# Kernel tuning notes

Measured on AMD Instinct MI355X. Metric: run time of the kernel, lower is better.

Reference implementation:

```python
import jax, jax.numpy as jnp
import numpy as np

V, E, H, C = 50000, 300, 512, 3
B, P_LEN, H_LEN = 64, 128, 64


def _lstm(x, Wih, Whh, bih, bhh, h0, c0):
    """torch-style LSTM (gate order i,f,g,o). x: [B,T,E] -> outputs [B,T,H], hT, cT."""
    def step(carry, xt):
        h, c = carry
        g = xt @ Wih.T + h @ Whh.T + bih + bhh  # [B,4H]
        i, f, gg, o = jnp.split(g, 4, axis=-1)
        c = jax.nn.sigmoid(f) * c + jax.nn.sigmoid(i) * jnp.tanh(gg)
        h = jax.nn.sigmoid(o) * jnp.tanh(c)
        return (h, c), h
    (hT, cT), ys = jax.lax.scan(step, (h0, c0), jnp.swapaxes(x, 0, 1))
    return jnp.swapaxes(ys, 0, 1), hT, cT


def setup_inputs() -> dict:
    key = jax.random.key(0)
    ks = iter(jax.random.split(key, 32))
    n = lambda shape, s=0.05: jax.random.normal(next(ks), shape, dtype=jnp.float32) * s
    inp = {
        "premise": jax.random.randint(next(ks), (B, P_LEN), 0, V, dtype=jnp.int32),
        "hypothesis": jax.random.randint(next(ks), (B, H_LEN), 0, V, dtype=jnp.int32),
        "emb": n((V, E), 0.1),
        "Wih1": n((4 * H, E)), "Whh1": n((4 * H, H)), "bih1": n((4 * H,)), "bhh1": n((4 * H,)),
        "Wih2": n((4 * H, E)), "Whh2": n((4 * H, H)), "bih2": n((4 * H,)), "bhh2": n((4 * H,)),
        "W_y": n((H, H)), "W_h": n((H, H)), "W_r": n((H, H)), "W_t": n((H, H)),
        "w_att": n((1, H)),
        "fc1_w": n((H, H)), "fc1_b": n((H,)),
        "fc2_w": n((H, H)), "fc2_b": n((H,)),
        "fc3_w": n((C, H)), "fc3_b": n((C,)),
    }
    return inp


def reference(premise, hypothesis, emb,
              Wih1, Whh1, bih1, bhh1,
              Wih2, Whh2, bih2, bhh2,
              W_y, W_h, W_r, W_t, w_att,
              fc1_w, fc1_b, fc2_w, fc2_b, fc3_w, fc3_b):
    Bsz = premise.shape[0]
    Hd = Whh1.shape[1]
    zeros = jnp.zeros((Bsz, Hd), jnp.float32)

    # premise LSTM
    xp = emb[premise]                                   # [B,P,E]
    out_p, _, c_p = _lstm(xp, Wih1, Whh1, bih1, bhh1, zeros, zeros)
    # hypothesis LSTM initialized with (h0=0, c0=c_p)
    xh = emb[hypothesis]                                # [B,Th,E]
    out_h, hn_h, _ = _lstm(xh, Wih2, Whh2, bih2, bhh2, zeros, c_p)

    # word-by-word attention: a1 = W_y @ V^T, fixed across steps
    a1 = jnp.einsum('hj,bpj->bhp', W_y, out_p)          # [B,H,P]
    wv = w_att[0]                                       # [H]

    def att_step(r, q_t):
        # r: [B,H] attention state; q_t: [B,H] hypothesis step
        a2 = q_t @ W_h.T + r @ W_r.T                    # [B,H]
        s = jnp.einsum('h,bhp->bp', wv, jnp.tanh(a1 + a2[:, :, None]))
        scores = jax.nn.softmax(s, axis=-1)             # over premise positions
        r = jnp.einsum('bph,bp->bh', out_p, scores) + jnp.tanh(r @ W_t.T)
        return r, None

    r, _ = jax.lax.scan(att_step, zeros, jnp.swapaxes(out_h, 0, 1))

    rep = jnp.tanh(r @ fc1_w.T + fc1_b + hn_h @ fc2_w.T + fc2_b)
    return rep @ fc3_w.T + fc3_b                         # [B,C]
```

## Files before the change

kernel.cpp:

```cpp
#include <hip/hip_runtime.h>
#include <math.h>

#define BSZ 64
#define PLEN 128
#define HLEN 64
#define EDIM 300
#define HDIM 512
#define G4 2048
#define NCLS 3

#define SPIN_CAP (1 << 18)

#define CR16 576
#define C16(f) ((((f) >> 5) * 36) + ((f) & 31))

__device__ __forceinline__ float sigf(float x) { return 1.0f / (1.0f + __expf(-x)); }
__device__ __forceinline__ float tanhfast(float x) { return 1.0f - 2.0f / (__expf(2.0f * x) + 1.0f); }

__device__ __forceinline__ unsigned long long aload64(const unsigned long long* p) {
    return __hip_atomic_load(p, __ATOMIC_RELAXED, __HIP_MEMORY_SCOPE_AGENT);
}
__device__ __forceinline__ void astore64(unsigned long long* p, unsigned long long v) {
    __hip_atomic_store(p, v, __ATOMIC_RELAXED, __HIP_MEMORY_SCOPE_AGENT);
}
__device__ __forceinline__ unsigned long long fpack2(float lo, float hi) {
    float2 v = make_float2(lo, hi);
    return *(unsigned long long*)&v;
}
__device__ __forceinline__ float2 funpack2(unsigned long long u) {
    union { unsigned long long u; float2 f; } c; c.u = u; return c.f;
}

__global__ __launch_bounds__(256) void ws_zero(unsigned long long* p) {
    p[(size_t)blockIdx.x * 256 + threadIdx.x] = 0ull;
}

__global__ __launch_bounds__(256) void proj_kernel(
    const int* __restrict__ toks, const float* __restrict__ emb,
    const float* __restrict__ Wih, const float* __restrict__ bih,
    const float* __restrict__ bhh, float* __restrict__ out)
{
    __shared__ float es[32 * 100];
    __shared__ float wsh[64 * 100];
    __shared__ int tks[32];
    const int m0 = blockIdx.x * 32, r0 = blockIdx.y * 64;
    const int tid = threadIdx.x;
    const int tx = tid & 15, ty = tid >> 4;
    float acc[2][4] = {{0.f, 0.f, 0.f, 0.f}, {0.f, 0.f, 0.f, 0.f}};
    if (tid < 32) tks[tid] = toks[m0 + tid];
    __syncthreads();
    for (int kc = 0; kc < 3; kc++) {
        if (kc) __syncthreads();
        for (int i = tid; i < 800; i += 256) {
            int row = i / 25, k4 = i % 25;
            ((float4*)es)[i] = ((const float4*)(emb + (size_t)tks[row] * EDIM + kc * 100))[k4];
        }
        for (int i = tid; i < 1600; i += 256) {
            int row = i / 25, k4 = i % 25;
            ((float4*)wsh)[i] = ((const float4*)(Wih + (size_t)(r0 + row) * EDIM + kc * 100))[k4];
        }
        __syncthreads();
        const float4* e0 = (const float4*)es + ty * 25;
        const float4* e1 = e0 + 16 * 25;
        const float4* w0 = (const float4*)wsh + tx * 25;
#pragma unroll
        for (int k = 0; k < 25; k++) {
            float4 ea = e0[k], eb = e1[k];
#pragma unroll
            for (int j = 0; j < 4; j++) {
                float4 w = w0[k + j * 400];
                acc[0][j] += ea.x * w.x + ea.y * w.y + ea.z * w.z + ea.w * w.w;
                acc[1][j] += eb.x * w.x + eb.y * w.y + eb.z * w.z + eb.w * w.w;
            }
        }
    }
#pragma unroll
    for (int j = 0; j < 4; j++) {
        int rr = r0 + tx + j * 16;
        float bsum = bih[rr] + bhh[rr];
        out[(size_t)(m0 + ty) * G4 + rr]      = acc[0][j] + bsum;
        out[(size_t)(m0 + ty + 16) * G4 + rr] = acc[1][j] + bsum;
    }
}

__global__ __launch_bounds__(256, 1) void lstm_coop(
    const float* __restrict__ xp, const float* __restrict__ xh,
    const float* __restrict__ Whh1, const float* __restrict__ Whh2,
    float* __restrict__ outp, float* __restrict__ outh,
    unsigned long long* __restrict__ hA, unsigned long long* __restrict__ hB,
    unsigned long long* __restrict__ hC, unsigned long long* __restrict__ hD,
    unsigned long long* __restrict__ doneH)
{
    const int tid = threadIdx.x;
    const int ug = blockIdx.x >> 3;
    const int bg = blockIdx.x & 7;
    const int u0 = ug * 16, b0 = bg * 8;
    const int rq = tid >> 4, cc = tid & 15;

    __shared__ __align__(16) float hst[8 * CR16];
    __shared__ float gsm[64][9];

    float4 w4[32];
#pragma unroll
    for (int j = 0; j < 4; j++) {
        int rr = 4 * rq + j;
        const float4* src = (const float4*)(Whh1 +
            ((size_t)((rr >> 4) * HDIM + u0 + (rr & 15))) * HDIM) + cc * 8;
#pragma unroll
        for (int q = 0; q < 8; q++) w4[j * 8 + q] = src[q];
    }
    float creg = 0.0f;
    const int bbc = tid >> 4, uuc = tid & 15;
    unsigned long long* dn = doneH + bg * 32;

    for (int t = 0; t < PLEN + HLEN; t++) {
        const int layer2 = (t >= PLEN) ? 1 : 0;
        const int tloc = layer2 ? t - PLEN : t;
        const int T = layer2 ? HLEN : PLEN;
        const float* xproj = layer2 ? xh : xp;
        float* outseq = layer2 ? outh : outp;
        unsigned long long* wA = layer2 ? hC : hA;
        unsigned long long* wB = layer2 ? hD : hB;
        unsigned long long* hwr = (t & 1) ? wB : wA;
        const unsigned long long* hrd = (t & 1) ? wA : wB;

        float gi = 0.f, gf = 0.f, gg = 0.f, go = 0.f;
        if (tid < 128) {
            size_t xb = ((size_t)(b0 + bbc) * T + tloc) * G4 + u0 + uuc;
            gi = xproj[xb];        gf = xproj[xb + 512];
            gg = xproj[xb + 1024]; go = xproj[xb + 1536];
        }

        if (t == PLEN) {
#pragma unroll
            for (int j = 0; j < 4; j++) {
                int rr = 4 * rq + j;
                const float4* src = (const float4*)(Whh2 +
                    ((size_t)((rr >> 4) * HDIM + u0 + (rr & 15))) * HDIM) + cc * 8;
#pragma unroll
                for (int q = 0; q < 8; q++) w4[j * 8 + q] = src[q];
            }
        }
        const bool have_h = (tloc != 0);
        if (have_h) {
            if (tid < 32) {
                unsigned long long v = aload64(dn + tid);
                int guard = 0;
                while (!__all(v >= (unsigned long long)t)) {
                    if (++guard > SPIN_CAP) break;
                    __builtin_amdgcn_s_sleep(1);
                    if (v < (unsigned long long)t) v = aload64(dn + tid);
                }
            }
            __syncthreads();
            __asm__ volatile("" ::: "memory");
            const unsigned long long* src = hrd + (size_t)b0 * 256;
            unsigned long long v[8];
#pragma unroll
            for (int i = 0; i < 8; i++) v[i] = aload64(src + tid + i * 256);
#pragma unroll
            for (int i = 0; i < 8; i++) {
                int idx = tid + i * 256;
                int bb = idx >> 8, j = idx & 255;
                float2 f = funpack2(v[i]);
                *(float2*)&hst[bb * CR16 + C16(2 * j)] = f;
            }
            __syncthreads();
#pragma unroll 1
            for (int bb = 0; bb < 8; bb++) {
                const float* hb = &hst[bb * CR16 + cc * 36];
                float a0 = 0.f, a1 = 0.f, a2 = 0.f, a3 = 0.f;
#pragma unroll
                for (int q = 0; q < 8; q++) {
                    float4 hv = *(const float4*)(hb + 4 * q);
                    float4 x;
                    x = w4[q];      a0 += x.x * hv.x + x.y * hv.y + x.z * hv.z + x.w * hv.w;
                    x = w4[8 + q];  a1 += x.x * hv.x + x.y * hv.y + x.z * hv.z + x.w * hv.w;
                    x = w4[16 + q]; a2 += x.x * hv.x + x.y * hv.y + x.z * hv.z + x.w * hv.w;
                    x = w4[24 + q]; a3 += x.x * hv.x + x.y * hv.y + x.z * hv.z + x.w * hv.w;
                }
#pragma unroll
                for (int o = 1; o < 16; o <<= 1) {
                    a0 += __shfl_xor(a0, o);
                    a1 += __shfl_xor(a1, o);
                    a2 += __shfl_xor(a2, o);
                    a3 += __shfl_xor(a3, o);
                }
                if (cc == 0) {
                    gsm[4 * rq + 0][bb] = a0;
                    gsm[4 * rq + 1][bb] = a1;
                    gsm[4 * rq + 2][bb] = a2;
                    gsm[4 * rq + 3][bb] = a3;
                }
            }
        }
        __syncthreads();
        float hn = 0.f;
        if (tid < 128) {
            if (have_h) {
                gi += gsm[uuc][bbc];
                gf += gsm[16 + uuc][bbc];
                gg += gsm[32 + uuc][bbc];
                go += gsm[48 + uuc][bbc];
            }
            float cn = sigf(gf) * creg + sigf(gi) * tanhfast(gg);
            hn = sigf(go) * tanhfast(cn);
            creg = cn;
            float pr = __shfl_xor(hn, 1);
            if ((uuc & 1) == 0)
                astore64(hwr + (size_t)(b0 + bbc) * 256 + (u0 + uuc) / 2, fpack2(hn, pr));
        }
        __asm__ volatile("s_waitcnt vmcnt(0)" ::: "memory");
        __syncthreads();
        if (tid == 0) astore64(&dn[ug], (unsigned long long)(t + 1));
        if (tid < 128)
            outseq[((size_t)(b0 + bbc) * T + tloc) * HDIM + u0 + uuc] = hn;
    }
}

__global__ __launch_bounds__(256) void a1_kernel(
    const float* __restrict__ W, const float* __restrict__ src,
    float* __restrict__ dst, int T)
{
    __shared__ float os[32 * 132];
    __shared__ float wsh[64 * 132];
    const int b = blockIdx.x, p0 = blockIdx.y * 32, h0 = blockIdx.z * 64;
    const int tid = threadIdx.x;
    const int tx = tid & 15, ty = tid >> 4;
    float acc[2][4] = {{0.f, 0.f, 0.f, 0.f}, {0.f, 0.f, 0.f, 0.f}};
    for (int kc = 0; kc < 4; kc++) {
        if (kc) __syncthreads();
        for (int i = tid; i < 1024; i += 256) {
            int row = i >> 5, k4 = i & 31;
            ((float4*)os)[row * 33 + k4] =
                ((const float4*)(src + ((size_t)(b * T) + p0 + row) * HDIM + kc * 128))[k4];
        }
        for (int i = tid; i < 2048; i += 256) {
            int row = i >> 5, k4 = i & 31;
            ((float4*)wsh)[row * 33 + k4] =
                ((const float4*)(W + (size_t)(h0 + row) * HDIM + kc * 128))[k4];
        }
        __syncthreads();
        const float4* o0 = (const float4*)os + ty * 33;
        const float4* o1 = o0 + 16 * 33;
        const float4* w0 = (const float4*)wsh + tx * 33;
#pragma unroll
        for (int k = 0; k < 32; k++) {
            float4 ea = o0[k], eb = o1[k];
#pragma unroll
            for (int j = 0; j < 4; j++) {
                float4 w = w0[k + j * 528];
                acc[0][j] += ea.x * w.x + ea.y * w.y + ea.z * w.z + ea.w * w.w;
                acc[1][j] += eb.x * w.x + eb.y * w.y + eb.z * w.z + eb.w * w.w;
            }
        }
    }
#pragma unroll
    for (int j = 0; j < 4; j++) {
        int hh = h0 + tx + j * 16;
        dst[((size_t)b * T + p0 + ty) * HDIM + hh]      = acc[0][j];
        dst[((size_t)b * T + p0 + ty + 16) * HDIM + hh] = acc[1][j];
    }
}

#define OSTR 2056
__global__ __launch_bounds__(256, 1) void att_coop2(
    const float* __restrict__ a1b,
    const float* __restrict__ a2qb,
    const float* __restrict__ outp,
    const float* __restrict__ Wr, const float* __restrict__ Wt,
    const float* __restrict__ wv,
    unsigned long long* __restrict__ rA, unsigned long long* __restrict__ rB,
    unsigned long long* __restrict__ sPart,
    unsigned long long* __restrict__ dnS, unsigned long long* __restrict__ dnR)
{
    const int tid = threadIdx.x;
    const int ug = blockIdx.x >> 3;
    const int bg = blockIdx.x & 7;
    const int u0 = ug * 16, b0 = bg * 8;
    const int rp = tid >> 4, cc = tid & 15;
    const int ab = tid >> 5, aq = tid & 31;

    __shared__ __align__(16) float rst[8 * CR16];
    __shared__ __align__(16) float ops[8 * OSTR];
    __shared__ __align__(16) float scst[8][132];
    __shared__ float a2sl[16][9];
    __shared__ float ttsl[16][9];
    __shared__ float wvs[16];

    float4 wr4[8], wt4[8];
    {
        const float4* sr = (const float4*)(Wr + (size_t)(u0 + rp) * HDIM) + cc * 8;
        const float4* st = (const float4*)(Wt + (size_t)(u0 + rp) * HDIM) + cc * 8;
#pragma unroll
        for (int q = 0; q < 8; q++) { wr4[q] = sr[q]; wt4[q] = st[q]; }
    }
    if (tid < 16) wvs[tid] = wv[u0 + tid];

    for (int i = tid; i < 8 * 128 * 4; i += 256) {
        int bb = i >> 9;
        int rem = i & 511;
        int p = rem >> 2, q = rem & 3;
        float4 v = *((const float4*)(outp + ((size_t)(b0 + bb) * PLEN + p) * HDIM + u0) + q);
        *((float4*)(ops + bb * OSTR + p * 16) + q) = v;
    }
    float4 a1r[4][4];
#pragma unroll
    for (int p = 0; p < 4; p++) {
        const float4* src = (const float4*)(a1b +
            ((size_t)(b0 + ab) * PLEN + 4 * aq + p) * HDIM + u0);
#pragma unroll
        for (int k = 0; k < 4; k++) a1r[p][k] = src[k];
    }
    __syncthreads();

    unsigned long long* myS = dnS + bg * 32;
    unsigned long long* myR = dnR + bg * 32;
    const int bbc = tid >> 4, uuc = tid & 15;

    for (int t = 0; t < HLEN; t++) {
        unsigned long long* rwr = (t & 1) ? rB : rA;
        const unsigned long long* rrd = (t & 1) ? rA : rB;
        unsigned long long* sp = sPart + ((size_t)((t & 1) * 8 + bg)) * 16384;

        if (tid < 128) {
            int b = tid >> 4, hh = tid & 15;
            a2sl[hh][b] = a2qb[((size_t)(b0 + b) * HLEN + t) * HDIM + u0 + hh];
            ttsl[hh][b] = 0.f;
        }
        if (t > 0) {
            if (tid < 32) {
                unsigned long long v = aload64(myR + tid);
                int guard = 0;
                while (!__all(v >= (unsigned long long)t)) {
                    if (++guard > SPIN_CAP) break;
                    __builtin_amdgcn_s_sleep(1);
                    if (v < (unsigned long long)t) v = aload64(myR + tid);
                }
            }
            __syncthreads();
            __asm__ volatile("" ::: "memory");
            const unsigned long long* src = rrd + (size_t)b0 * 256;
            unsigned long long v[8];
#pragma unroll
            for (int i = 0; i < 8; i++) v[i] = aload64(src + tid + i * 256);
#pragma unroll
            for (int i = 0; i < 8; i++) {
                int idx = tid + i * 256;
                int bb = idx >> 8, j = idx & 255;
                float2 f = funpack2(v[i]);
                *(float2*)&rst[bb * CR16 + C16(2 * j)] = f;
            }
        }
        __syncthreads();
        if (t > 0) {
#pragma unroll 1
            for (int b = 0; b < 8; b++) {
                const float* hb = &rst[b * CR16 + cc * 36];
                float ar = 0.f, at = 0.f;
#pragma unroll
                for (int q = 0; q < 8; q++) {
                    float4 hv = *(const float4*)(hb + 4 * q);
                    float4 x = wr4[q], y = wt4[q];
                    ar += x.x * hv.x + x.y * hv.y + x.z * hv.z + x.w * hv.w;
                    at += y.x * hv.x + y.y * hv.y + y.z * hv.z + y.w * hv.w;
                }
#pragma unroll
                for (int o = 1; o < 16; o <<= 1) {
                    ar += __shfl_xor(ar, o);
                    at += __shfl_xor(at, o);
                }
                if (cc == 0) {
                    a2sl[rp][b] += ar;
                    ttsl[rp][b] = tanhfast(at);
                }
            }
        }
        __syncthreads();
        {
            float s4[4];
#pragma unroll
            for (int p = 0; p < 4; p++) {
                float s = 0.f;
#pragma unroll
                for (int k = 0; k < 4; k++) {
                    float4 av = a1r[p][k];
                    s += wvs[4 * k + 0] * tanhfast(av.x + a2sl[4 * k + 0][ab])
                       + wvs[4 * k + 1] * tanhfast(av.y + a2sl[4 * k + 1][ab])
                       + wvs[4 * k + 2] * tanhfast(av.z + a2sl[4 * k + 2][ab])
                       + wvs[4 * k + 3] * tanhfast(av.w + a2sl[4 * k + 3][ab]);
                }
                s4[p] = s;
            }
            unsigned long long* d = sp + ((size_t)ug * 8 + ab) * 64 + aq * 2;
            astore64(d, fpack2(s4[0], s4[1]));
            astore64(d + 1, fpack2(s4[2], s4[3]));
        }
        __asm__ volatile("s_waitcnt vmcnt(0)" ::: "memory");
        __syncthreads();
        if (tid == 0) astore64(&myS[ug], (unsigned long long)(t + 1));

        {
            if (tid < 32) {
                unsigned long long v = aload64(myS + tid);
                int guard = 0;
                while (!__all(v >= (unsigned long long)(t + 1))) {
                    if (++guard > SPIN_CAP) break;
                    __builtin_amdgcn_s_sleep(1);
                    if (v < (unsigned long long)(t + 1)) v = aload64(myS + tid);
                }
            }
            __syncthreads();
            __asm__ volatile("" ::: "memory");
#pragma unroll
            for (int i = 0; i < 2; i++) {
                int idx = tid + i * 256;
                int b = idx >> 6, p2 = idx & 63;
                float sx = 0.f, sy = 0.f;
#pragma unroll 8
                for (int g = 0; g < 32; g++) {
                    float2 f = funpack2(aload64(sp + ((size_t)g * 8 + b) * 64 + p2));
                    sx += f.x; sy += f.y;
                }
                scst[b][2 * p2] = sx;
                scst[b][2 * p2 + 1] = sy;
            }
        }
        __syncthreads();
        {
            const int bb = tid >> 5, j = tid & 31;
            float4 v = *(float4*)&scst[bb][j * 4];
            float mx = fmaxf(fmaxf(v.x, v.y), fmaxf(v.z, v.w));
#pragma unroll
            for (int o = 1; o < 32; o <<= 1) mx = fmaxf(mx, __shfl_xor(mx, o));
            float ex = __expf(v.x - mx), ey = __expf(v.y - mx);
            float ez = __expf(v.z - mx), ew = __expf(v.w - mx);
            float ssum = (ex + ey) + (ez + ew);
#pragma unroll
            for (int o = 1; o < 32; o <<= 1) ssum += __shfl_xor(ssum, o);
            float inv = 1.0f / ssum;
            float4 sc4 = make_float4(ex * inv, ey * inv, ez * inv, ew * inv);
            *(float4*)&scst[bb][j * 4] = sc4;
        }
        __syncthreads();
        if (tid < 128) {
            float acc = ttsl[uuc][bbc];
            const float* opb = ops + bbc * OSTR + uuc;
#pragma unroll 8
            for (int p = 0; p < PLEN; p++)
                acc += scst[bbc][p] * opb[p * 16];
            float pr = __shfl_xor(acc, 1);
            if ((uuc & 1) == 0)
                astore64(rwr + (size_t)(b0 + bbc) * 256 + (u0 + uuc) / 2, fpack2(acc, pr));
        }
        __asm__ volatile("s_waitcnt vmcnt(0)" ::: "memory");
        __syncthreads();
        if (tid == 0) astore64(&myR[ug], (unsigned long long)(t + 1));
    }
}

__global__ __launch_bounds__(256) void final_kernel(
    const unsigned long long* __restrict__ r2, const float* __restrict__ outh,
    const float* __restrict__ fc1w, const float* __restrict__ fc1b,
    const float* __restrict__ fc2w, const float* __restrict__ fc2b,
    const float* __restrict__ fc3w, const float* __restrict__ fc3b,
    float* __restrict__ out)
{
    int b = blockIdx.x, tid = threadIdx.x;
    __shared__ float rs[HDIM], hs[HDIM], rep[HDIM], red[256];
    {
        float2 f = funpack2(r2[(size_t)b * 256 + tid]);
        rs[2 * tid] = f.x; rs[2 * tid + 1] = f.y;
    }
    for (int i = tid; i < 128; i += 256)
        ((float4*)hs)[i] = ((const float4*)(outh + ((size_t)(b * HLEN + HLEN - 1)) * HDIM))[i];
    __syncthreads();
    for (int u = tid; u < HDIM; u += 256) {
        const float4* w1 = (const float4*)(fc1w + (size_t)u * HDIM);
        const float4* w2 = (const float4*)(fc2w + (size_t)u * HDIM);
        float a = 0.f, bacc = 0.f;
        for (int k = 0; k < 128; k++) {
            float4 rv = ((float4*)rs)[k], hv = ((float4*)hs)[k];
            float4 x = w1[k]; a    += rv.x * x.x + rv.y * x.y + rv.z * x.z + rv.w * x.w;
            float4 y = w2[k]; bacc += hv.x * y.x + hv.y * y.y + hv.z * y.z + hv.w * y.w;
        }
        rep[u] = tanhfast(a + fc1b[u] + bacc + fc2b[u]);
    }
    __syncthreads();
    for (int cix = 0; cix < NCLS; cix++) {
        red[tid] = rep[tid] * fc3w[(size_t)cix * HDIM + tid]
                 + rep[tid + 256] * fc3w[(size_t)cix * HDIM + tid + 256];
        __syncthreads();
        for (int off = 128; off; off >>= 1) {
            if (tid < off) red[tid] += red[tid + off];
            __syncthreads();
        }
        if (tid == 0) out[b * NCLS + cix] = red[0] + fc3b[cix];
        __syncthreads();
    }
}

extern "C" void kernel_launch(void* const* d_in, const int* in_sizes, int n_in,
                              void* d_out, int out_size, void* d_ws, size_t ws_size,
                              hipStream_t stream)
{
    const int*   premise = (const int*)d_in[0];
    const int*   hyp     = (const int*)d_in[1];
    const float* emb     = (const float*)d_in[2];
    const float* Wih1    = (const float*)d_in[3];
    const float* Whh1    = (const float*)d_in[4];
    const float* bih1    = (const float*)d_in[5];
    const float* bhh1    = (const float*)d_in[6];
    const float* Wih2    = (const float*)d_in[7];
    const float* Whh2    = (const float*)d_in[8];
    const float* bih2    = (const float*)d_in[9];
    const float* bhh2    = (const float*)d_in[10];
    const float* Wy      = (const float*)d_in[11];
    const float* Wh      = (const float*)d_in[12];
    const float* Wr      = (const float*)d_in[13];
    const float* Wt      = (const float*)d_in[14];
    const float* wv      = (const float*)d_in[15];
    const float* fc1w    = (const float*)d_in[16];
    const float* fc1b    = (const float*)d_in[17];
    const float* fc2w    = (const float*)d_in[18];
    const float* fc2b    = (const float*)d_in[19];
    const float* fc3w    = (const float*)d_in[20];
    const float* fc3b    = (const float*)d_in[21];
    float* out = (float*)d_out;

    float* ws = (float*)d_ws;
    size_t off = 0;
    float* xp    = ws + off; off += (size_t)BSZ * PLEN * G4;
    float* xh    = ws + off; off += (size_t)BSZ * HLEN * G4;
    float* outp  = ws + off; off += (size_t)BSZ * PLEN * HDIM;
    float* outhp = ws + off; off += (size_t)BSZ * HLEN * HDIM;
    float* a1b   = ws + off; off += (size_t)BSZ * HDIM * PLEN;
    float* a2qb  = xp;
    unsigned long long* tbase = (unsigned long long*)(ws + off);
    unsigned long long* hAb   = tbase;
    unsigned long long* hBb   = tbase + 16384;
    unsigned long long* hCb   = tbase + 2 * 16384;
    unsigned long long* hDb   = tbase + 3 * 16384;
    unsigned long long* sPart = tbase + 4 * 16384;
    unsigned long long* dnH   = sPart + 262144;
    unsigned long long* dnS   = dnH + 256;
    unsigned long long* dnR   = dnS + 256;
    off += (size_t)(4 * 16384 + 262144 + 768) * 2;
    if (ws_size < off * sizeof(float)) return;

    ws_zero<<<dim3(3), dim3(256), 0, stream>>>(dnH);

    proj_kernel<<<dim3(BSZ * PLEN / 32, G4 / 64), dim3(256), 0, stream>>>(
        premise, emb, Wih1, bih1, bhh1, xp);
    proj_kernel<<<dim3(BSZ * HLEN / 32, G4 / 64), dim3(256), 0, stream>>>(
        hyp, emb, Wih2, bih2, bhh2, xh);

    lstm_coop<<<dim3(256), dim3(256), 0, stream>>>(
        xp, xh, Whh1, Whh2, outp, outhp, hAb, hBb, hCb, hDb, dnH);

    a1_kernel<<<dim3(BSZ, PLEN / 32, HDIM / 64), dim3(256), 0, stream>>>(
        Wy, outp, a1b, PLEN);
    a1_kernel<<<dim3(BSZ, HLEN / 32, HDIM / 64), dim3(256), 0, stream>>>(
        Wh, outhp, a2qb, HLEN);

    att_coop2<<<dim3(256), dim3(256), 0, stream>>>(
        a1b, a2qb, outp, Wr, Wt, wv, hCb, hDb, sPart, dnS, dnR);

    final_kernel<<<dim3(BSZ), dim3(256), 0, stream>>>(
        hDb, outhp, fc1w, fc1b, fc2w, fc2b, fc3w, fc3b, out);
}
```

Before: 3.141 ms.

## Fuse LSTM and attention into one persistent kernel with streamed a1/a2 computation

New measurement: 3.233 ms. 2.9% more time.

```diff
diff --git a/kernel.cpp b/kernel.cpp
--- a/kernel.cpp
+++ b/kernel.cpp
@@ -21,6 +21,12 @@
     return __hip_atomic_load(p, __ATOMIC_RELAXED, __HIP_MEMORY_SCOPE_AGENT);
 }
 __device__ __forceinline__ void astore64(unsigned long long* p, unsigned long long v) {
+    __hip_atomic_store(p, v, __ATOMIC_RELAXED, __HIP_MEMORY_SCOPE_AGENT);
+}
+__device__ __forceinline__ float aload32f(const float* p) {
+    return __hip_atomic_load(p, __ATOMIC_RELAXED, __HIP_MEMORY_SCOPE_AGENT);
+}
+__device__ __forceinline__ void astore32f(float* p, float v) {
     __hip_atomic_store(p, v, __ATOMIC_RELAXED, __HIP_MEMORY_SCOPE_AGENT);
 }
 __device__ __forceinline__ unsigned long long fpack2(float lo, float hi) {
@@ -83,263 +89,275 @@
     }
 }
 
-__global__ __launch_bounds__(256, 1) void lstm_coop(
+__global__ __launch_bounds__(256, 2) void fused_coop(
     const float* __restrict__ xp, const float* __restrict__ xh,
     const float* __restrict__ Whh1, const float* __restrict__ Whh2,
     float* __restrict__ outp, float* __restrict__ outh,
     unsigned long long* __restrict__ hA, unsigned long long* __restrict__ hB,
     unsigned long long* __restrict__ hC, unsigned long long* __restrict__ hD,
-    unsigned long long* __restrict__ doneH)
-{
-    const int tid = threadIdx.x;
-    const int ug = blockIdx.x >> 3;
-    const int bg = blockIdx.x & 7;
-    const int u0 = ug * 16, b0 = bg * 8;
-    const int rq = tid >> 4, cc = tid & 15;
-
-    __shared__ __align__(16) float hst[8 * CR16];
-    __shared__ float gsm[64][9];
-
-    float4 w4[32];
-#pragma unroll
-    for (int j = 0; j < 4; j++) {
-        int rr = 4 * rq + j;
-        const float4* src = (const float4*)(Whh1 +
-            ((size_t)((rr >> 4) * HDIM + u0 + (rr & 15))) * HDIM) + cc * 8;
-#pragma unroll
-        for (int q = 0; q < 8; q++) w4[j * 8 + q] = src[q];
-    }
-    float creg = 0.0f;
-    const int bbc = tid >> 4, uuc = tid & 15;
-    unsigned long long* dn = doneH + bg * 32;
-
-    for (int t = 0; t < PLEN + HLEN; t++) {
-        const int layer2 = (t >= PLEN) ? 1 : 0;
-        const int tloc = layer2 ? t - PLEN : t;
-        const int T = layer2 ? HLEN : PLEN;
-        const float* xproj = layer2 ? xh : xp;
-        float* outseq = layer2 ? outh : outp;
-        unsigned long long* wA = layer2 ? hC : hA;
-        unsigned long long* wB = layer2 ? hD : hB;
-        unsigned long long* hwr = (t & 1) ? wB : wA;
-        const unsigned long long* hrd = (t & 1) ? wA : wB;
-
-        float gi = 0.f, gf = 0.f, gg = 0.f, go = 0.f;
-        if (tid < 128) {
-            size_t xb = ((size_t)(b0 + bbc) * T + tloc) * G4 + u0 + uuc;
-            gi = xproj[xb];        gf = xproj[xb + 512];
-            gg = xproj[xb + 1024]; go = xproj[xb + 1536];
-        }
-
-        if (t == PLEN) {
-#pragma unroll
-            for (int j = 0; j < 4; j++) {
-                int rr = 4 * rq + j;
-                const float4* src = (const float4*)(Whh2 +
-                    ((size_t)((rr >> 4) * HDIM + u0 + (rr & 15))) * HDIM) + cc * 8;
-#pragma unroll
-                for (int q = 0; q < 8; q++) w4[j * 8 + q] = src[q];
-            }
-        }
-        const bool have_h = (tloc != 0);
-        if (have_h) {
-            if (tid < 32) {
-                unsigned long long v = aload64(dn + tid);
-                int guard = 0;
-                while (!__all(v >= (unsigned long long)t)) {
-                    if (++guard > SPIN_CAP) break;
-                    __builtin_amdgcn_s_sleep(1);
-                    if (v < (unsigned long long)t) v = aload64(dn + tid);
-                }
-            }
-            __syncthreads();
-            __asm__ volatile("" ::: "memory");
-            const unsigned long long* src = hrd + (size_t)b0 * 256;
-            unsigned long long v[8];
-#pragma unroll
-            for (int i = 0; i < 8; i++) v[i] = aload64(src + tid + i * 256);
-#pragma unroll
-            for (int i = 0; i < 8; i++) {
-                int idx = tid + i * 256;
-                int bb = idx >> 8, j = idx & 255;
-                float2 f = funpack2(v[i]);
-                *(float2*)&hst[bb * CR16 + C16(2 * j)] = f;
-            }
-            __syncthreads();
-#pragma unroll 1
-            for (int bb = 0; bb < 8; bb++) {
-                const float* hb = &hst[bb * CR16 + cc * 36];
-                float a0 = 0.f, a1 = 0.f, a2 = 0.f, a3 = 0.f;
-#pragma unroll
-                for (int q = 0; q < 8; q++) {
-                    float4 hv = *(const float4*)(hb + 4 * q);
-                    float4 x;
-                    x = w4[q];      a0 += x.x * hv.x + x.y * hv.y + x.z * hv.z + x.w * hv.w;
-                    x = w4[8 + q];  a1 += x.x * hv.x + x.y * hv.y + x.z * hv.z + x.w * hv.w;
-                    x = w4[16 + q]; a2 += x.x * hv.x + x.y * hv.y + x.z * hv.z + x.w * hv.w;
-                    x = w4[24 + q]; a3 += x.x * hv.x + x.y * hv.y + x.z * hv.z + x.w * hv.w;
-                }
-#pragma unroll
-                for (int o = 1; o < 16; o <<= 1) {
-                    a0 += __shfl_xor(a0, o);
-                    a1 += __shfl_xor(a1, o);
-                    a2 += __shfl_xor(a2, o);
-                    a3 += __shfl_xor(a3, o);
-                }
-                if (cc == 0) {
-                    gsm[4 * rq + 0][bb] = a0;
-                    gsm[4 * rq + 1][bb] = a1;
-                    gsm[4 * rq + 2][bb] = a2;
-                    gsm[4 * rq + 3][bb] = a3;
-                }
-            }
-        }
-        __syncthreads();
-        float hn = 0.f;
-        if (tid < 128) {
-            if (have_h) {
-                gi += gsm[uuc][bbc];
-                gf += gsm[16 + uuc][bbc];
-                gg += gsm[32 + uuc][bbc];
-                go += gsm[48 + uuc][bbc];
-            }
-            float cn = sigf(gf) * creg + sigf(gi) * tanhfast(gg);
-            hn = sigf(go) * tanhfast(cn);
-            creg = cn;
-            float pr = __shfl_xor(hn, 1);
-            if ((uuc & 1) == 0)
-                astore64(hwr + (size_t)(b0 + bbc) * 256 + (u0 + uuc) / 2, fpack2(hn, pr));
-        }
-        __asm__ volatile("s_waitcnt vmcnt(0)" ::: "memory");
-        __syncthreads();
-        if (tid == 0) astore64(&dn[ug], (unsigned long long)(t + 1));
-        if (tid < 128)
-            outseq[((size_t)(b0 + bbc) * T + tloc) * HDIM + u0 + uuc] = hn;
-    }
-}
-
-__global__ __launch_bounds__(256) void a1_kernel(
-    const float* __restrict__ W, const float* __restrict__ src,
-    float* __restrict__ dst, int T)
-{
-    __shared__ float os[32 * 132];
-    __shared__ float wsh[64 * 132];
-    const int b = blockIdx.x, p0 = blockIdx.y * 32, h0 = blockIdx.z * 64;
-    const int tid = threadIdx.x;
-    const int tx = tid & 15, ty = tid >> 4;
-    float acc[2][4] = {{0.f, 0.f, 0.f, 0.f}, {0.f, 0.f, 0.f, 0.f}};
-    for (int kc = 0; kc < 4; kc++) {
-        if (kc) __syncthreads();
-        for (int i = tid; i < 1024; i += 256) {
-            int row = i >> 5, k4 = i & 31;
-            ((float4*)os)[row * 33 + k4] =
-                ((const float4*)(src + ((size_t)(b * T) + p0 + row) * HDIM + kc * 128))[k4];
-        }
-        for (int i = tid; i < 2048; i += 256) {
-            int row = i >> 5, k4 = i & 31;
-            ((float4*)wsh)[row * 33 + k4] =
-                ((const float4*)(W + (size_t)(h0 + row) * HDIM + kc * 128))[k4];
-        }
-        __syncthreads();
-        const float4* o0 = (const float4*)os + ty * 33;
-        const float4* o1 = o0 + 16 * 33;
-        const float4* w0 = (const float4*)wsh + tx * 33;
-#pragma unroll
-        for (int k = 0; k < 32; k++) {
-            float4 ea = o0[k], eb = o1[k];
-#pragma unroll
-            for (int j = 0; j < 4; j++) {
-                float4 w = w0[k + j * 528];
-                acc[0][j] += ea.x * w.x + ea.y * w.y + ea.z * w.z + ea.w * w.w;
-                acc[1][j] += eb.x * w.x + eb.y * w.y + eb.z * w.z + eb.w * w.w;
-            }
-        }
-    }
-#pragma unroll
-    for (int j = 0; j < 4; j++) {
-        int hh = h0 + tx + j * 16;
-        dst[((size_t)b * T + p0 + ty) * HDIM + hh]      = acc[0][j];
-        dst[((size_t)b * T + p0 + ty + 16) * HDIM + hh] = acc[1][j];
-    }
-}
-
-#define OSTR 2056
-__global__ __launch_bounds__(256, 1) void att_coop2(
-    const float* __restrict__ a1b,
-    const float* __restrict__ a2qb,
-    const float* __restrict__ outp,
-    const float* __restrict__ Wr, const float* __restrict__ Wt,
+    unsigned long long* __restrict__ doneH,
+    float* __restrict__ a1b,
+    const float* __restrict__ Wh, const float* __restrict__ Wr,
+    const float* __restrict__ Wt, const float* __restrict__ Wy,
     const float* __restrict__ wv,
     unsigned long long* __restrict__ rA, unsigned long long* __restrict__ rB,
     unsigned long long* __restrict__ sPart,
     unsigned long long* __restrict__ dnS, unsigned long long* __restrict__ dnR)
 {
+    extern __shared__ __align__(16) float smem[];
     const int tid = threadIdx.x;
-    const int ug = blockIdx.x >> 3;
-    const int bg = blockIdx.x & 7;
+
+    if (blockIdx.x < 256) {
+        const int ug = blockIdx.x >> 3;
+        const int bg = blockIdx.x & 7;
+        const int u0 = ug * 16, b0 = bg * 8;
+        const int rq = tid >> 4, cc = tid & 15;
+
+        float* hst = smem;
+        float* gsm = smem + 8 * CR16;
+
+        float4 w4[32];
+#pragma unroll
+        for (int j = 0; j < 4; j++) {
+            int rr = 4 * rq + j;
+            const float4* src = (const float4*)(Whh1 +
+                ((size_t)((rr >> 4) * HDIM + u0 + (rr & 15))) * HDIM) + cc * 8;
+#pragma unroll
+            for (int q = 0; q < 8; q++) w4[j * 8 + q] = src[q];
+        }
+        float creg = 0.0f;
+        const int bbc = tid >> 4, uuc = tid & 15;
+        unsigned long long* dn = doneH + bg * 32;
+
+        for (int t = 0; t < PLEN + HLEN; t++) {
+            const int layer2 = (t >= PLEN) ? 1 : 0;
+            const int tloc = layer2 ? t - PLEN : t;
+            const int T = layer2 ? HLEN : PLEN;
+            const float* xproj = layer2 ? xh : xp;
+            float* outseq = layer2 ? outh : outp;
+            unsigned long long* wA = layer2 ? hC : hA;
+            unsigned long long* wB = layer2 ? hD : hB;
+            unsigned long long* hwr = (t & 1) ? wB : wA;
+            const unsigned long long* hrd = (t & 1) ? wA : wB;
+
+            float gi = 0.f, gf = 0.f, gg = 0.f, go = 0.f;
+            if (tid < 128) {
+                size_t xb = ((size_t)(b0 + bbc) * T + tloc) * G4 + u0 + uuc;
+                gi = xproj[xb];        gf = xproj[xb + 512];
+                gg = xproj[xb + 1024]; go = xproj[xb + 1536];
+            }
+            if (t == PLEN) {
+#pragma unroll
+                for (int j = 0; j < 4; j++) {
+                    int rr = 4 * rq + j;
+                    const float4* src = (const float4*)(Whh2 +
+                        ((size_t)((rr >> 4) * HDIM + u0 + (rr & 15))) * HDIM) + cc * 8;
+#pragma unroll
+                    for (int q = 0; q < 8; q++) w4[j * 8 + q] = src[q];
+                }
+            }
+            const bool have_h = (tloc != 0);
+            if (have_h) {
+                if (tid < 32) {
+                    unsigned long long v = aload64(dn + tid);
+                    int guard = 0;
+                    while (!__all(v >= (unsigned long long)t)) {
+                        if (++guard > SPIN_CAP) break;
+                        __builtin_amdgcn_s_sleep(1);
+                        if (v < (unsigned long long)t) v = aload64(dn + tid);
+                    }
+                }
+                __syncthreads();
+                __asm__ volatile("" ::: "memory");
+                const unsigned long long* src = hrd + (size_t)b0 * 256;
+                unsigned long long v[8];
+#pragma unroll
+                for (int i = 0; i < 8; i++) v[i] = aload64(src + tid + i * 256);
+#pragma unroll
+                for (int i = 0; i < 8; i++) {
+                    int idx = tid + i * 256;
+                    int bb = idx >> 8, j = idx & 255;
+                    float2 f = funpack2(v[i]);
+                    *(float2*)&hst[bb * CR16 + C16(2 * j)] = f;
+                }
+                __syncthreads();
+#pragma unroll 1
+                for (int bb = 0; bb < 8; bb++) {
+                    const float* hb = &hst[bb * CR16 + cc * 36];
+                    float a0 = 0.f, a1 = 0.f, a2 = 0.f, a3 = 0.f;
+#pragma unroll
+                    for (int q = 0; q < 8; q++) {
+                        float4 hv = *(const float4*)(hb + 4 * q);
+                        float4 x;
+                        x = w4[q];      a0 += x.x * hv.x + x.y * hv.y + x.z * hv.z + x.w * hv.w;
+                        x = w4[8 + q];  a1 += x.x * hv.x + x.y * hv.y + x.z * hv.z + x.w * hv.w;
+                        x = w4[16 + q]; a2 += x.x * hv.x + x.y * hv.y + x.z * hv.z + x.w * hv.w;
+                        x = w4[24 + q]; a3 += x.x * hv.x + x.y * hv.y + x.z * hv.z + x.w * hv.w;
+                    }
+#pragma unroll
+                    for (int o = 1; o < 16; o <<= 1) {
+                        a0 += __shfl_xor(a0, o);
+                        a1 += __shfl_xor(a1, o);
+                        a2 += __shfl_xor(a2, o);
+                        a3 += __shfl_xor(a3, o);
+                    }
+                    if (cc == 0) {
+                        gsm[(4 * rq + 0) * 9 + bb] = a0;
+                        gsm[(4 * rq + 1) * 9 + bb] = a1;
+                        gsm[(4 * rq + 2) * 9 + bb] = a2;
+                        gsm[(4 * rq + 3) * 9 + bb] = a3;
+                    }
+                }
+            }
+            __syncthreads();
+            if (tid < 128) {
+                if (have_h) {
+                    gi += gsm[uuc * 9 + bbc];
+                    gf += gsm[(16 + uuc) * 9 + bbc];
+                    gg += gsm[(32 + uuc) * 9 + bbc];
+                    go += gsm[(48 + uuc) * 9 + bbc];
+                }
+                float cn = sigf(gf) * creg + sigf(gi) * tanhfast(gg);
+                float hn = sigf(go) * tanhfast(cn);
+                creg = cn;
+                float pr = __shfl_xor(hn, 1);
+                if ((uuc & 1) == 0)
+                    astore64(hwr + (size_t)(b0 + bbc) * 256 + (u0 + uuc) / 2, fpack2(hn, pr));
+                astore32f(outseq + ((size_t)(b0 + bbc) * T + tloc) * HDIM + u0 + uuc, hn);
+            }
+            __asm__ volatile("s_waitcnt vmcnt(0)" ::: "memory");
+            __syncthreads();
+            if (tid == 0) astore64(&dn[ug], (unsigned long long)(t + 1));
+        }
+        return;
+    }
+
+    const int local = blockIdx.x - 256;
+    const int ug = local >> 3;
+    const int bg = local & 7;
     const int u0 = ug * 16, b0 = bg * 8;
     const int rp = tid >> 4, cc = tid & 15;
     const int ab = tid >> 5, aq = tid & 31;
 
-    __shared__ __align__(16) float rst[8 * CR16];
-    __shared__ __align__(16) float ops[8 * OSTR];
-    __shared__ __align__(16) float scst[8][132];
-    __shared__ float a2sl[16][9];
-    __shared__ float ttsl[16][9];
-    __shared__ float wvs[16];
-
-    float4 wr4[8], wt4[8];
+    float* qst  = smem;
+    float* rst  = smem + 4608;
+    float* scst = smem + 9216;
+    float* a2sl = smem + 10272;
+    float* ttsl = smem + 10416;
+    float* wvs  = smem + 10560;
+    float* psum = smem + 10576;
+
+    float4 wh4[8], wr4[8], wt4[8];
     {
+        const float4* sh = (const float4*)(Wh + (size_t)(u0 + rp) * HDIM) + cc * 8;
         const float4* sr = (const float4*)(Wr + (size_t)(u0 + rp) * HDIM) + cc * 8;
         const float4* st = (const float4*)(Wt + (size_t)(u0 + rp) * HDIM) + cc * 8;
 #pragma unroll
-        for (int q = 0; q < 8; q++) { wr4[q] = sr[q]; wt4[q] = st[q]; }
+        for (int q = 0; q < 8; q++) { wh4[q] = sh[q]; wr4[q] = sr[q]; wt4[q] = st[q]; }
     }
     if (tid < 16) wvs[tid] = wv[u0 + tid];
 
-    for (int i = tid; i < 8 * 128 * 4; i += 256) {
-        int bb = i >> 9;
-        int rem = i & 511;
-        int p = rem >> 2, q = rem & 3;
-        float4 v = *((const float4*)(outp + ((size_t)(b0 + bb) * PLEN + p) * HDIM + u0) + q);
-        *((float4*)(ops + bb * OSTR + p * 16) + q) = v;
-    }
-    float4 a1r[4][4];
-#pragma unroll
-    for (int p = 0; p < 4; p++) {
-        const float4* src = (const float4*)(a1b +
-            ((size_t)(b0 + ab) * PLEN + 4 * aq + p) * HDIM + u0);
-#pragma unroll
-        for (int k = 0; k < 4; k++) a1r[p][k] = src[k];
-    }
-    __syncthreads();
-
+    unsigned long long* dnl = doneH + bg * 32;
     unsigned long long* myS = dnS + bg * 32;
     unsigned long long* myR = dnR + bg * 32;
     const int bbc = tid >> 4, uuc = tid & 15;
+
+    {
+        float4 wy4[8];
+        const float4* sy = (const float4*)(Wy + (size_t)(u0 + rp) * HDIM) + cc * 8;
+#pragma unroll
+        for (int q = 0; q < 8; q++) wy4[q] = sy[q];
+
+        for (int p = 0; p < PLEN; p++) {
+            if (tid < 32) {
+                unsigned long long v = aload64(dnl + tid);
+                int guard = 0;
+                while (!__all(v >= (unsigned long long)(p + 1))) {
+                    if (++guard > SPIN_CAP) break;
+                    __builtin_amdgcn_s_sleep(1);
+                    if (v < (unsigned long long)(p + 1)) v = aload64(dnl + tid);
+                }
+            }
+            __syncthreads();
+            __asm__ volatile("" ::: "memory");
+            {
+                const unsigned long long* src =
+                    (const unsigned long long*)(outp) + ((size_t)b0 * PLEN + p) * 256;
+#pragma unroll
+                for (int i = 0; i < 8; i++) {
+                    int idx = tid + i * 256;
+                    int bb = idx >> 8, j = idx & 255;
+                    float2 f = funpack2(aload64(src + (size_t)bb * PLEN * 256 + j));
+                    *(float2*)&qst[bb * CR16 + C16(2 * j)] = f;
+                }
+            }
+            __syncthreads();
+#pragma unroll 1
+            for (int b = 0; b < 8; b++) {
+                const float* qb = &qst[b * CR16 + cc * 36];
+                float a = 0.f;
+#pragma unroll
+                for (int q = 0; q < 8; q++) {
+                    float4 qv = *(const float4*)(qb + 4 * q);
+                    float4 x = wy4[q];
+                    a += x.x * qv.x + x.y * qv.y + x.z * qv.z + x.w * qv.w;
+                }
+#pragma unroll
+                for (int o = 1; o < 16; o <<= 1) a += __shfl_xor(a, o);
+                if (cc == 0)
+                    a1b[((size_t)(b0 + b) * PLEN + p) * HDIM + u0 + rp] = a;
+            }
+            __syncthreads();
+        }
+    }
+    __asm__ volatile("s_waitcnt vmcnt(0)" ::: "memory");
+    __syncthreads();
+    float4 a1r[4][4];
+#pragma unroll
+    for (int pi = 0; pi < 4; pi++) {
+        const float4* src = (const float4*)(a1b +
+            ((size_t)(b0 + ab) * PLEN + 4 * aq + pi) * HDIM + u0);
+#pragma unroll
+        for (int k = 0; k < 4; k++) a1r[pi][k] = src[k];
+    }
 
     for (int t = 0; t < HLEN; t++) {
         unsigned long long* rwr = (t & 1) ? rB : rA;
         const unsigned long long* rrd = (t & 1) ? rA : rB;
         unsigned long long* sp = sPart + ((size_t)((t & 1) * 8 + bg)) * 16384;
 
-        if (tid < 128) {
-            int b = tid >> 4, hh = tid & 15;
-            a2sl[hh][b] = a2qb[((size_t)(b0 + b) * HLEN + t) * HDIM + u0 + hh];
-            ttsl[hh][b] = 0.f;
+        if (tid < 32) {
+            unsigned long long v = aload64(dnl + tid);
+            int guard = 0;
+            while (!__all(v >= (unsigned long long)(129 + t))) {
+                if (++guard > SPIN_CAP) break;
+                __builtin_amdgcn_s_sleep(1);
+                if (v < (unsigned long long)(129 + t)) v = aload64(dnl + tid);
+            }
+        }
+        if (t > 0 && tid < 32) {
+            unsigned long long v = aload64(myR + tid);
+            int guard = 0;
+            while (!__all(v >= (unsigned long long)t)) {
+                if (++guard > SPIN_CAP) break;
+                __builtin_amdgcn_s_sleep(1);
+                if (v < (unsigned long long)t) v = aload64(myR + tid);
+            }
+        }
+        __syncthreads();
+        __asm__ volatile("" ::: "memory");
+        {
+            const unsigned long long* src =
+                (const unsigned long long*)(outh) + ((size_t)b0 * HLEN + t) * 256;
+#pragma unroll
+            for (int i = 0; i < 8; i++) {
+                int idx = tid + i * 256;
+                int bb = idx >> 8, j = idx & 255;
+                float2 f = funpack2(aload64(src + (size_t)bb * HLEN * 256 + j));
+                *(float2*)&qst[bb * CR16 + C16(2 * j)] = f;
+            }
         }
         if (t > 0) {
-            if (tid < 32) {
-                unsigned long long v = aload64(myR + tid);
-                int guard = 0;
-                while (!__all(v >= (unsigned long long)t)) {
-                    if (++guard > SPIN_CAP) break;
-                    __builtin_amdgcn_s_sleep(1);
-                    if (v < (unsigned long long)t) v = aload64(myR + tid);
-                }
-            }
-            __syncthreads();
-            __asm__ volatile("" ::: "memory");
             const unsigned long long* src = rrd + (size_t)b0 * 256;
             unsigned long long v[8];
 #pragma unroll
@@ -356,23 +374,45 @@
         if (t > 0) {
 #pragma unroll 1
             for (int b = 0; b < 8; b++) {
-                const float* hb = &rst[b * CR16 + cc * 36];
-                float ar = 0.f, at = 0.f;
+                const float* qb = &qst[b * CR16 + cc * 36];
+                const float* rb = &rst[b * CR16 + cc * 36];
+                float ah = 0.f, ar = 0.f, at = 0.f;
 #pragma unroll
                 for (int q = 0; q < 8; q++) {
-                    float4 hv = *(const float4*)(hb + 4 * q);
-                    float4 x = wr4[q], y = wt4[q];
-                    ar += x.x * hv.x + x.y * hv.y + x.z * hv.z + x.w * hv.w;
-                    at += y.x * hv.x + y.y * hv.y + y.z * hv.z + y.w * hv.w;
-                }
+                    float4 qv = *(const float4*)(qb + 4 * q);
+                    float4 rv = *(const float4*)(rb + 4 * q);
+                    float4 x = wh4[q], y = wr4[q], z = wt4[q];
+                    ah += x.x * qv.x + x.y * qv.y + x.z * qv.z + x.w * qv.w;
+                    ar += y.x * rv.x + y.y * rv.y + y.z * rv.z + y.w * rv.w;
+                    at += z.x * rv.x + z.y * rv.y + z.z * rv.z + z.w * rv.w;
+                }
+                float a2v = ah + ar;
 #pragma unroll
                 for (int o = 1; o < 16; o <<= 1) {
-                    ar += __shfl_xor(ar, o);
-                    at += __shfl_xor(at, o);
+                    a2v += __shfl_xor(a2v, o);
+                    at  += __shfl_xor(at, o);
                 }
                 if (cc == 0) {
-                    a2sl[rp][b] += ar;
-                    ttsl[rp][b] = tanhfast(at);
+                    a2sl[rp * 9 + b] = a2v;
+                    ttsl[rp * 9 + b] = tanhfast(at);
+                }
+            }
+        } else {
+#pragma unroll 1
+            for (int b = 0; b < 8; b++) {
+                const float* qb = &qst[b * CR16 + cc * 36];
+                float ah = 0.f;
+#pragma unroll
+                for (int q = 0; q < 8; q++) {
+                    float4 qv = *(const float4*)(qb + 4 * q);
+                    float4 x = wh4[q];
+                    ah += x.x * qv.x + x.y * qv.y + x.z * qv.z + x.w * qv.w;
+                }
+#pragma unroll
+                for (int o = 1; o < 16; o <<= 1) ah += __shfl_xor(ah, o);
+                if (cc == 0) {
+                    a2sl[rp * 9 + b] = ah;
+                    ttsl[rp * 9 + b] = 0.f;
                 }
             }
         }
@@ -380,17 +420,17 @@
         {
             float s4[4];
 #pragma unroll
-            for (int p = 0; p < 4; p++) {
+            for (int pi = 0; pi < 4; pi++) {
                 float s = 0.f;
 #pragma unroll
                 for (int k = 0; k < 4; k++) {
-                    float4 av = a1r[p][k];
-                    s += wvs[4 * k + 0] * tanhfast(av.x + a2sl[4 * k + 0][ab])
-                       + wvs[4 * k + 1] * tanhfast(av.y + a2sl[4 * k + 1][ab])
-                       + wvs[4 * k + 2] * tanhfast(av.z + a2sl[4 * k + 2][ab])
-                       + wvs[4 * k + 3] * tanhfast(av.w + a2sl[4 * k + 3][ab]);
-                }
-                s4[p] = s;
+                    float4 av = a1r[pi][k];
+                    s += wvs[4 * k + 0] * tanhfast(av.x + a2sl[(4 * k + 0) * 9 + ab])
+                       + wvs[4 * k + 1] * tanhfast(av.y + a2sl[(4 * k + 1) * 9 + ab])
+                       + wvs[4 * k + 2] * tanhfast(av.z + a2sl[(4 * k + 2) * 9 + ab])
+                       + wvs[4 * k + 3] * tanhfast(av.w + a2sl[(4 * k + 3) * 9 + ab]);
+                }
+                s4[pi] = s;
             }
             unsigned long long* d = sp + ((size_t)ug * 8 + ab) * 64 + aq * 2;
             astore64(d, fpack2(s4[0], s4[1]));
@@ -422,14 +462,14 @@
                     float2 f = funpack2(aload64(sp + ((size_t)g * 8 + b) * 64 + p2));
                     sx += f.x; sy += f.y;
                 }
-                scst[b][2 * p2] = sx;
-                scst[b][2 * p2 + 1] = sy;
+                scst[b * 132 + 2 * p2] = sx;
+                scst[b * 132 + 2 * p2 + 1] = sy;
             }
         }
         __syncthreads();
         {
             const int bb = tid >> 5, j = tid & 31;
-            float4 v = *(float4*)&scst[bb][j * 4];
+            float4 v = *(float4*)&scst[bb * 132 + j * 4];
             float mx = fmaxf(fmaxf(v.x, v.y), fmaxf(v.z, v.w));
 #pragma unroll
             for (int o = 1; o < 32; o <<= 1) mx = fmaxf(mx, __shfl_xor(mx, o));
@@ -440,15 +480,22 @@
             for (int o = 1; o < 32; o <<= 1) ssum += __shfl_xor(ssum, o);
             float inv = 1.0f / ssum;
             float4 sc4 = make_float4(ex * inv, ey * inv, ez * inv, ew * inv);
-            *(float4*)&scst[bb][j * 4] = sc4;
+            *(float4*)&scst[bb * 132 + j * 4] = sc4;
+        }
+        __syncthreads();
+        {
+            const int ph = tid >> 7, pair = tid & 127;
+            const int b2 = pair >> 4, u2 = pair & 15;
+            float acc = (ph == 0) ? ttsl[u2 * 9 + b2] : 0.f;
+            const float* opb = outp + ((size_t)(b0 + b2) * PLEN + ph * 64) * HDIM + u0 + u2;
+#pragma unroll 8
+            for (int p = 0; p < 64; p++)
+                acc += scst[b2 * 132 + ph * 64 + p] * aload32f(opb + (size_t)p * HDIM);
+            psum[tid] = acc;
         }
         __syncthreads();
         if (tid < 128) {
-            float acc = ttsl[uuc][bbc];
-            const float* opb = ops + bbc * OSTR + uuc;
-#pragma unroll 8
-            for (int p = 0; p < PLEN; p++)
-                acc += scst[bbc][p] * opb[p * 16];
+            float acc = psum[tid] + psum[tid + 128];
             float pr = __shfl_xor(acc, 1);
             if ((uuc & 1) == 0)
                 astore64(rwr + (size_t)(b0 + bbc) * 256 + (u0 + uuc) / 2, fpack2(acc, pr));
@@ -535,17 +582,18 @@
     float* outp  = ws + off; off += (size_t)BSZ * PLEN * HDIM;
     float* outhp = ws + off; off += (size_t)BSZ * HLEN * HDIM;
     float* a1b   = ws + off; off += (size_t)BSZ * HDIM * PLEN;
-    float* a2qb  = xp;
     unsigned long long* tbase = (unsigned long long*)(ws + off);
     unsigned long long* hAb   = tbase;
     unsigned long long* hBb   = tbase + 16384;
     unsigned long long* hCb   = tbase + 2 * 16384;
     unsigned long long* hDb   = tbase + 3 * 16384;
-    unsigned long long* sPart = tbase + 4 * 16384;
+    unsigned long long* rAtt  = tbase + 4 * 16384;
+    unsigned long long* rBtt  = tbase + 5 * 16384;
+    unsigned long long* sPart = tbase + 6 * 16384;
     unsigned long long* dnH   = sPart + 262144;
     unsigned long long* dnS   = dnH + 256;
     unsigned long long* dnR   = dnS + 256;
-    off += (size_t)(4 * 16384 + 262144 + 768) * 2;
+    off += (size_t)(6 * 16384 + 262144 + 768) * 2;
     if (ws_size < off * sizeof(float)) return;
 
     ws_zero<<<dim3(3), dim3(256), 0, stream>>>(dnH);
@@ -555,17 +603,12 @@
     proj_kernel<<<dim3(BSZ * HLEN / 32, G4 / 64), dim3(256), 0, stream>>>(
         hyp, emb, Wih2, bih2, bhh2, xh);
 
-    lstm_coop<<<dim3(256), dim3(256), 0, stream>>>(
-        xp, xh, Whh1, Whh2, outp, outhp, hAb, hBb, hCb, hDb, dnH);
-
-    a1_kernel<<<dim3(BSZ, PLEN / 32, HDIM / 64), dim3(256), 0, stream>>>(
-        Wy, outp, a1b, PLEN);
-    a1_kernel<<<dim3(BSZ, HLEN / 32, HDIM / 64), dim3(256), 0, stream>>>(
-        Wh, outhp, a2qb, HLEN);
-
-    att_coop2<<<dim3(256), dim3(256), 0, stream>>>(
-        a1b, a2qb, outp, Wr, Wt, wv, hCb, hDb, sPart, dnS, dnR);
+    fused_coop<<<dim3(512), dim3(256), 43328, stream>>>(
+        xp, xh, Whh1, Whh2, outp, outhp,
+        hAb, hBb, hCb, hDb, dnH,
+        a1b, Wh, Wr, Wt, Wy, wv,
+        rAtt, rBtt, sPart, dnS, dnR);
 
     final_kernel<<<dim3(BSZ), dim3(256), 0, stream>>>(
-        hDb, outhp, fc1w, fc1b, fc2w, fc2b, fc3w, fc3b, out);
-}
+        rBtt, outhp, fc1w, fc1b, fc2w, fc2b, fc3w, fc3b, out);
+}
```
